# Kernel optimization log

Hardware: AMD Instinct MI355X
Metric: run time of the kernel (lower is better)

Reference implementation:

```python
import jax, jax.numpy as jnp
import numpy as np
from jax import lax

DIM, HID, NH, KD, D, WH = 256, 512, 4, 16, 64, 7


def _conv(x, w, pad, groups):
    return lax.conv_general_dilated(
        x, w, (1, 1), [(pad, pad), (pad, pad)],
        dimension_numbers=('NCHW', 'OIHW', 'NCHW'), feature_group_count=groups)


def _conv_bn(x, w, s, b, pad=0, groups=1):
    # Conv2d(bias=False) followed by eval-mode BatchNorm folded to per-channel affine
    y = _conv(x, w, pad, groups)
    return y * s[None, :, None, None] + b[None, :, None, None]


def _ffn(x, w1, s1, b1, w2, s2, b2):
    return _conv_bn(jax.nn.relu(_conv_bn(x, w1, s1, b1)), w2, s2, b2)


def _window(t, c, B, H, W):
    # [B,NH,c,H,W] -> [B,NH,H//WH,W//WH,WH*WH,c]
    t = t.reshape(B, NH, c, H // WH, WH, W // WH, WH)
    t = t.transpose(0, 1, 3, 5, 4, 6, 2)
    return t.reshape(B, NH, H // WH, W // WH, WH * WH, c)


def _local_window_attn(x, qkv_w, qkv_s, qkv_b, dws_w, dws_s, dws_b,
                       proj_w, proj_s, proj_b, pos_emb):
    B, C, H, W = x.shape
    scale = KD ** -0.5
    qkv = _conv_bn(x, qkv_w, qkv_s, qkv_b)          # [B, NH*(2KD+D), H, W]
    qkv = qkv.reshape(B, NH, 2 * KD + D, H, W)
    q, k, v = qkv[:, :, :KD], qkv[:, :, KD:2 * KD], qkv[:, :, 2 * KD:]
    # per-head depthwise 5x5 conv on q
    q = jax.vmap(lambda qi, wi, si, bi: _conv_bn(qi, wi, si, bi, pad=2, groups=KD),
                 in_axes=(1, 0, 0, 0), out_axes=1)(q, dws_w, dws_s, dws_b)
    q = _window(q, KD, B, H, W)
    k = _window(k, KD, B, H, W)
    v = _window(v, D, B, H, W)
    attn = jnp.einsum('bhijqc,bhijkc->bhijqk', q, k) * scale \
        + pos_emb[None, :, None, None]               # [B,NH,nWh,nWw,Ws,Ws]
    attn = jax.nn.softmax(attn, axis=-1)
    o = jnp.einsum('bhijqk,bhijkd->bhijqd', attn, v)
    o = o.reshape(B, NH, H // WH, W // WH, WH, WH, D)
    o = o.transpose(0, 1, 6, 2, 4, 3, 5).reshape(B, NH * D, H, W)
    return _conv_bn(jax.nn.relu(o), proj_w, proj_s, proj_b)


def setup_inputs() -> dict:
    key = jax.random.key(0)
    ks = iter(jax.random.split(key, 40))
    n = lambda shp, sc=0.05: jax.random.normal(next(ks), shp, jnp.float32) * sc
    u = lambda shp: jax.random.uniform(next(ks), shp, jnp.float32, minval=0.5, maxval=1.5)
    inp = {'x': jax.random.normal(next(ks), (64, DIM, 28, 28), jnp.float32)}
    for p in ('dw0', 'dw1'):
        inp[p + '_w'] = n((DIM, 1, 3, 3))
        inp[p + '_s'] = u((DIM,))
        inp[p + '_b'] = n((DIM,))
    for p in ('ffn0', 'ffn1'):
        inp[p + '_w1'] = n((HID, DIM, 1, 1))
        inp[p + '_s1'] = u((HID,))
        inp[p + '_b1'] = n((HID,))
        inp[p + '_w2'] = n((DIM, HID, 1, 1))
        inp[p + '_s2'] = u((DIM,))
        inp[p + '_b2'] = n((DIM,))
    inp['qkv_w'] = n((NH * (2 * KD + D), DIM, 1, 1))
    inp['qkv_s'] = u((NH * (2 * KD + D),))
    inp['qkv_b'] = n((NH * (2 * KD + D),))
    inp['dws_w'] = n((NH, KD, 1, 5, 5))
    inp['dws_s'] = u((NH, KD))
    inp['dws_b'] = n((NH, KD))
    inp['proj_w'] = n((DIM, NH * D, 1, 1))
    inp['proj_s'] = u((DIM,))
    inp['proj_b'] = n((DIM,))
    inp['pos_emb'] = n((NH, WH * WH, WH * WH))
    return inp


def reference(x, dw0_w, dw0_s, dw0_b,
              ffn0_w1, ffn0_s1, ffn0_b1, ffn0_w2, ffn0_s2, ffn0_b2,
              qkv_w, qkv_s, qkv_b, dws_w, dws_s, dws_b,
              proj_w, proj_s, proj_b, pos_emb,
              dw1_w, dw1_s, dw1_b,
              ffn1_w1, ffn1_s1, ffn1_b1, ffn1_w2, ffn1_s2, ffn1_b2):
    x = x + _conv_bn(x, dw0_w, dw0_s, dw0_b, pad=1, groups=DIM)
    x = x + _ffn(x, ffn0_w1, ffn0_s1, ffn0_b1, ffn0_w2, ffn0_s2, ffn0_b2)
    x = x + _local_window_attn(x, qkv_w, qkv_s, qkv_b, dws_w, dws_s, dws_b,
                               proj_w, proj_s, proj_b, pos_emb)
    x = x + _conv_bn(x, dw1_w, dw1_s, dw1_b, pad=1, groups=DIM)
    x = x + _ffn(x, ffn1_w1, ffn1_s1, ffn1_b1, ffn1_w2, ffn1_s2, ffn1_b2)
    return x
```

## Files before the change

### kernel.cpp

```cpp
#include <hip/hip_runtime.h>
#include <hip/hip_bf16.h>
#include <math.h>

typedef __hip_bfloat16 bf16;
typedef __attribute__((ext_vector_type(8))) short short8;
typedef __attribute__((ext_vector_type(4))) float floatx4;

#define BB    64
#define DIMC  256
#define HIDC  512
#define NHH   4
#define HH_   28
#define WW_   28
#define PP    784

__device__ __forceinline__ float toF(bf16 x) { return __bfloat162float(x); }
__device__ __forceinline__ unsigned short f2bits(float f) {
    union { bf16 h; unsigned short u; } cv; cv.h = __float2bfloat16(f); return cv.u;
}
__device__ __forceinline__ float bits2f(unsigned short u) {
    union { unsigned int u32; float f; } cv; cv.u32 = ((unsigned int)u) << 16; return cv.f;
}

__device__ __forceinline__ void gll16(const void* g, void* l) {
    __builtin_amdgcn_global_load_lds(
        (const __attribute__((address_space(1))) void*)g,
        (__attribute__((address_space(3))) void*)l, 16, 0, 0);
}

__global__ __launch_bounds__(256) void cvt_all(
    const float* __restrict__ s0, bf16* __restrict__ d0,
    const float* __restrict__ s1, bf16* __restrict__ d1,
    const float* __restrict__ s2, bf16* __restrict__ d2,
    const float* __restrict__ s3, bf16* __restrict__ d3,
    const float* __restrict__ s4, bf16* __restrict__ d4,
    const float* __restrict__ s5, bf16* __restrict__ d5)
{
    int i = blockIdx.x * 256 + threadIdx.x;
    if (i < 131072)                d0[i]          = __float2bfloat16(s0[i]);
    else if (i < 262144)           d1[i - 131072] = __float2bfloat16(s1[i - 131072]);
    else if (i < 393216)           d2[i - 262144] = __float2bfloat16(s2[i - 262144]);
    else if (i < 524288)           d3[i - 393216] = __float2bfloat16(s3[i - 393216]);
    else if (i < 622592)           d4[i - 524288] = __float2bfloat16(s4[i - 524288]);
    else if (i < 688128)           d5[i - 622592] = __float2bfloat16(s5[i - 622592]);
}

#define CPB 4
__global__ __launch_bounds__(256) void dw3x3_kernel(
    const float* __restrict__ in, const float* __restrict__ w,
    const float* __restrict__ s, const float* __restrict__ b,
    float* __restrict__ out, bf16* __restrict__ outB)
{
    __shared__ float t[CPB][30 * 30];

    int wid = blockIdx.y * gridDim.x + blockIdx.x;
    int lin = (wid & 7) * 512 + (wid >> 3);
    int cg  = lin & 63;
    int n   = lin >> 6;
    int c0  = cg * CPB;

    int tid = threadIdx.x;
    int lm  = tid & 3;
    const float* ip = in  + ((size_t)n * DIMC + c0) * PP;
    float*       op = out + ((size_t)n * DIMC + c0) * PP;

    float w9[9];
#pragma unroll
    for (int i = 0; i < 9; i++) w9[i] = w[(c0 + lm) * 9 + i];
    float sc = s[c0 + lm], bb = b[c0 + lm];

    for (int i = tid; i < 464; i += 256) {
        int plane = i / 116, bq = i - plane * 116;
        int cell;
        if (bq < 30)       cell = bq;
        else if (bq < 60)  cell = 870 + (bq - 30);
        else if (bq < 88)  cell = (bq - 60 + 1) * 30;
        else               cell = (bq - 88 + 1) * 30 + 29;
        t[plane][cell] = 0.f;
    }
    for (int idx = tid; idx < CPB * 196; idx += 256) {
        int ch  = idx / 196;
        int rm  = idx - ch * 196;
        int row = rm / 7, seg = rm - row * 7;
        float4 v = *(const float4*)&ip[ch * PP + row * 28 + seg * 4];
        float* dst = &t[ch][(row + 1) * 30 + seg * 4 + 1];
        dst[0] = v.x; dst[1] = v.y; dst[2] = v.z; dst[3] = v.w;
    }
    __syncthreads();

    unsigned short* oBu = (unsigned short*)outB;
    for (int idx = tid; idx < CPB * 196; idx += 256) {
        int rm  = idx >> 2;
        int row = rm / 7, seg = rm - row * 7;
        int x0  = seg * 4;

        float acc[4] = {0.f, 0.f, 0.f, 0.f};
        float ctr[4];
        const float* base = &t[lm][row * 30 + x0];
#pragma unroll
        for (int i = 0; i < 3; i++) {
            float r[6];
#pragma unroll
            for (int k = 0; k < 6; k++) r[k] = base[i * 30 + k];
            if (i == 1) { ctr[0] = r[1]; ctr[1] = r[2]; ctr[2] = r[3]; ctr[3] = r[4]; }
#pragma unroll
            for (int j = 0; j < 3; j++)
#pragma unroll
                for (int q = 0; q < 4; q++)
                    acc[q] += w9[i * 3 + j] * r[j + q];
        }
        float v0 = ctr[0] + acc[0] * sc + bb;
        float v1 = ctr[1] + acc[1] * sc + bb;
        float v2 = ctr[2] + acc[2] * sc + bb;
        float v3 = ctr[3] + acc[3] * sc + bb;

        float4 o; o.x = v0; o.y = v1; o.z = v2; o.w = v3;
        *(float4*)&op[lm * PP + row * 28 + x0] = o;

        float ea = __shfl_xor((lm & 2) ? v0 : v2, 2);
        float eb = __shfl_xor((lm & 2) ? v1 : v3, 2);
        v0 = (lm & 2) ? ea : v0;  v1 = (lm & 2) ? eb : v1;
        v2 = (lm & 2) ? v2 : ea;  v3 = (lm & 2) ? v3 : eb;
        float ec = __shfl_xor((lm & 1) ? v0 : v1, 1);
        float ed = __shfl_xor((lm & 1) ? v2 : v3, 1);
        v0 = (lm & 1) ? ec : v0;  v1 = (lm & 1) ? v1 : ec;
        v2 = (lm & 1) ? ed : v2;  v3 = (lm & 1) ? v3 : ed;
        int p = row * 28 + x0 + lm;
        union { unsigned short h[4]; uint2 u; } pk;
        pk.h[0] = f2bits(v0); pk.h[1] = f2bits(v1);
        pk.h[2] = f2bits(v2); pk.h[3] = f2bits(v3);
        *(uint2*)&oBu[((size_t)n * PP + p) * DIMC + c0] = pk.u;
    }
}

__global__ __launch_bounds__(256) void dws5x5_nhwc(
    const bf16* __restrict__ qkv,
    const float* __restrict__ w,
    const float* __restrict__ s, const float* __restrict__ b,
    bf16* __restrict__ qout)
{
    __shared__ __align__(16) unsigned short qin[32 * 32 * 16];
    int hh  = blockIdx.x;
    int n   = blockIdx.y;
    int tid = threadIdx.x;
    const unsigned short* KVu = (const unsigned short*)qkv;

    int kcw = tid & 15;
    int hk  = hh * 16 + kcw;
    float w25[25];
#pragma unroll
    for (int i = 0; i < 25; i++) w25[i] = w[hk * 25 + i];
    float csc = s[hk], cbb = b[hk];

    for (int i = tid; i < 4096; i += 256)
        ((uint4*)qin)[i] = make_uint4(0u, 0u, 0u, 0u);
    __syncthreads();
    for (int idx = tid; idx < 1568; idx += 256) {
        int p = idx >> 1, half = idx & 1;
        int h = p / 28, x = p - h * 28;
        uint4 v = *(const uint4*)&KVu[((size_t)n * PP + p) * 384 + hh * 96 + half * 8];
        *(uint4*)&qin[((h + 2) * 32 + (x + 2)) * 16 + half * 8] = v;
    }
    __syncthreads();

    for (int idx = tid; idx < 12544; idx += 256) {
        int p = idx >> 4;
        int h = p / 28, x = p - h * 28;
        float acc = 0.f;
#pragma unroll
        for (int i = 0; i < 5; i++)
#pragma unroll
            for (int j = 0; j < 5; j++)
                acc += w25[i * 5 + j] * bits2f(qin[((h + i) * 32 + (x + j)) * 16 + kcw]);
        qout[((size_t)n * PP + p) * 64 + hk] = __float2bfloat16(acc * csc + cbb);
    }
}

template <bool RELU, bool RES, int OUTMODE>
__global__ __launch_bounds__(256) void gemm_mfma(
    const bf16* __restrict__ Wb,
    const bf16* __restrict__ X,
    const float* __restrict__ S, const float* __restrict__ Bb,
    const float* __restrict__ res,
    float* __restrict__ outF,
    bf16*  __restrict__ outB,
    int M, int K)
{
    int nwg = gridDim.x * gridDim.y * gridDim.z;
    int wid = (blockIdx.z * gridDim.y + blockIdx.y) * gridDim.x + blockIdx.x;
    int lin = (wid & 7) * (nwg >> 3) + (wid >> 3);
    int yb  = lin % gridDim.y;
    int t2  = lin / gridDim.y;
    int xb  = t2 % gridDim.x;
    int n   = t2 / gridDim.x;

    int co0  = yb * 64;
    int p0   = xb * 112;
    int tid  = threadIdx.x;
    int wv   = tid >> 6;
    int ln   = tid & 63;
    int l15  = ln & 15;
    int quad = ln >> 4;

    __shared__ __align__(16) unsigned short Blds[2][112 * 32];

    floatx4 acc[7];
#pragma unroll
    for (int t = 0; t < 7; t++) acc[t] = (floatx4){0.f, 0.f, 0.f, 0.f};

    const bf16* Arow = Wb + (size_t)(co0 + wv * 16 + l15) * K + quad * 8;
    const unsigned short* Xb = (const unsigned short*)X + ((size_t)n * PP + p0) * K;

    int rA = wv * 16 + (ln >> 2);
    int rB = 64 + wv * 16 + (ln >> 2);
    int cA = (ln & 3) ^ ((rA >> 1) & 3);
    int cB = (ln & 3) ^ ((rB >> 1) & 3);
    const unsigned short* gA = Xb + (size_t)rA * K + cA * 8;
    const unsigned short* gB = Xb + (size_t)rB * K + cB * 8;

    gll16(gA, &Blds[0][(wv * 16) * 32]);
    if (wv < 3) gll16(gB, &Blds[0][(64 + wv * 16) * 32]);
    short8 af = *(const short8*)Arow;
    __syncthreads();

    int NT = K >> 5;
    for (int t = 0; t < NT; t++) {
        int cur = t & 1;
        short8 naf = af;
        if (t + 1 < NT) {
            gll16(gA + (t + 1) * 32, &Blds[cur ^ 1][(wv * 16) * 32]);
            if (wv < 3) gll16(gB + (t + 1) * 32, &Blds[cur ^ 1][(64 + wv * 16) * 32]);
            naf = *(const short8*)(Arow + (t + 1) * 32);
        }
#pragma unroll
        for (int tt = 0; tt < 7; tt++) {
            int row = tt * 16 + l15;
            short8 bfrag = *(const short8*)
                &Blds[cur][row * 32 + ((quad ^ ((row >> 1) & 3)) * 8)];
            acc[tt] = __builtin_amdgcn_mfma_f32_16x16x32_bf16(af, bfrag, acc[tt], 0, 0, 0);
        }
        af = naf;
        __syncthreads();
    }

    int cobase = co0 + wv * 16 + quad * 4;
    float s4[4], b4[4];
#pragma unroll
    for (int r = 0; r < 4; r++) { s4[r] = S[cobase + r]; b4[r] = Bb[cobase + r]; }

#pragma unroll
    for (int t = 0; t < 7; t++) {
        int p = p0 + t * 16 + l15;
        float y[4];
#pragma unroll
        for (int r = 0; r < 4; r++) {
            y[r] = acc[t][r] * s4[r] + b4[r];
            if (RELU) y[r] = fmaxf(y[r], 0.f);
            if (RES) y[r] += res[((size_t)n * M + cobase + r) * PP + p];
        }
        if (OUTMODE == 1 || OUTMODE == 2) {
#pragma unroll
            for (int r = 0; r < 4; r++)
                outF[((size_t)n * M + cobase + r) * PP + p] = y[r];
        }
        if (OUTMODE == 0 || OUTMODE == 2) {
            union { unsigned short h4[4]; uint2 u; } pk;
#pragma unroll
            for (int r = 0; r < 4; r++) pk.h4[r] = f2bits(y[r]);
            *(uint2*)((unsigned short*)outB + ((size_t)n * PP + p) * M + cobase) = pk.u;
        }
    }
}

__global__ __launch_bounds__(256) void attn_kernel(
    const bf16*  __restrict__ Q,
    const bf16*  __restrict__ KV,
    const float* __restrict__ pos,
    bf16* __restrict__ O)
{
    int wjp = blockIdx.x & 1, wi = blockIdx.x >> 1;
    int hh  = blockIdx.y, n = blockIdx.z;
    int tid = threadIdx.x;
    int pbase = wi * 7 * 28 + wjp * 14;

    __shared__ __align__(16) char smem[51712];
    unsigned short* qS = (unsigned short*)smem;
    unsigned short* kS = qS + 2 * 64 * 40;
    unsigned short* pS = (unsigned short*)smem;
    unsigned short* vT = (unsigned short*)(smem + 20480);
    float*          posL = (float*)(smem + 20480 + 18432);

    const unsigned short* Qu  = (const unsigned short*)Q;
    const unsigned short* KVu = (const unsigned short*)KV;

    for (int idx = tid; idx < 1280; idx += 256) {
        int which = idx >= 640 ? 1 : 0;
        int t2 = idx - which * 640;
        int w = t2 / 320, rm = t2 - w * 320;
        int row = rm / 5, half = rm - row * 5;
        uint4 v = make_uint4(0u, 0u, 0u, 0u);
        if (row < 49 && half < 2) {
            int p = pbase + (row / 7) * 28 + w * 7 + (row % 7);
            const unsigned short* src = which
                ? &KVu[((size_t)n * PP + p) * 384 + hh * 96 + 16 + half * 8]
                : &Qu[((size_t)n * PP + p) * 64 + hh * 16 + half * 8];
            v = *(const uint4*)src;
        }
        *(uint4*)((which ? kS : qS) + (w * 64 + row) * 40 + half * 8) = v;
    }
    for (int idx = tid; idx < 1024; idx += 256) {
        int w = idx >> 9, rm = idx & 511;
        int ki = rm >> 3, dq = rm & 7;
        union { uint4 q; unsigned short h[8]; } v;
        v.q = make_uint4(0u, 0u, 0u, 0u);
        if (ki < 49) {
            int p = pbase + (ki / 7) * 28 + w * 7 + (ki % 7);
            v.q = *(const uint4*)&KVu[((size_t)n * PP + p) * 384 + hh * 96 + 32 + dq * 8];
        }
#pragma unroll
        for (int j = 0; j < 8; j++)
            vT[(w * 64 + dq * 8 + j) * 72 + ki] = v.h[j];
    }
    for (int idx = tid; idx < 3200; idx += 256) {
        int r = idx / 50, c = idx - r * 50;
        posL[idx] = (r < 49 && c < 49) ? pos[((size_t)hh * 49 + r) * 49 + c] : 0.f;
    }
    __syncthreads();

    int wv = tid >> 6, ln = tid & 63, l15 = ln & 15, quad = ln >> 4;

    uint2 pk[2][4];
#pragma unroll
    for (int w = 0; w < 2; w++) {
        short8 qf = *(const short8*)&qS[(w * 64 + wv * 16 + l15) * 40 + quad * 8];
        floatx4 a4[4];
#pragma unroll
        for (int kt = 0; kt < 4; kt++) {
            short8 kf = *(const short8*)&kS[(w * 64 + kt * 16 + l15) * 40 + quad * 8];
            a4[kt] = __builtin_amdgcn_mfma_f32_16x16x32_bf16(
                kf, qf, (floatx4){0.f, 0.f, 0.f, 0.f}, 0, 0, 0);
        }
        int q = wv * 16 + l15;
        float sv[16];
        float m = -1e30f;
#pragma unroll
        for (int kt = 0; kt < 4; kt++) {
#pragma unroll
            for (int r = 0; r < 4; r++) {
                int ki = kt * 16 + quad * 4 + r;
                float sc = (ki < 49)
                    ? a4[kt][r] * 0.25f + posL[q * 50 + ki]
                    : -1e30f;
                sv[kt * 4 + r] = sc;
                m = fmaxf(m, sc);
            }
        }
        m = fmaxf(m, __shfl_xor(m, 16));
        m = fmaxf(m, __shfl_xor(m, 32));
        float sum = 0.f;
#pragma unroll
        for (int i = 0; i < 16; i++) { sv[i] = __expf(sv[i] - m); sum += sv[i]; }
        sum += __shfl_xor(sum, 16);
        sum += __shfl_xor(sum, 32);
        float inv = 1.f / sum;
#pragma unroll
        for (int kt = 0; kt < 4; kt++) {
            union { uint2 u; unsigned short h[4]; } pku;
#pragma unroll
            for (int r = 0; r < 4; r++) pku.h[r] = f2bits(sv[kt * 4 + r] * inv);
            pk[w][kt] = pku.u;
        }
    }
    __syncthreads();

    {
        int q = wv * 16 + l15;
#pragma unroll
        for (int w = 0; w < 2; w++)
#pragma unroll
            for (int kt = 0; kt < 4; kt++)
                *(uint2*)&pS[(w * 64 + q) * 72 + kt * 16 + quad * 4] = pk[w][kt];
    }
    __syncthreads();

    unsigned short* Ou = (unsigned short*)O;
#pragma unroll
    for (int w = 0; w < 2; w++) {
        short8 af0 = *(const short8*)&pS[(w * 64 + wv * 16 + l15) * 72 + quad * 8];
        short8 af1 = *(const short8*)&pS[(w * 64 + wv * 16 + l15) * 72 + 32 + quad * 8];
#pragma unroll
        for (int dt = 0; dt < 4; dt++) {
            floatx4 oacc = (floatx4){0.f, 0.f, 0.f, 0.f};
            short8 vf0 = *(const short8*)&vT[(w * 64 + dt * 16 + l15) * 72 + quad * 8];
            short8 vf1 = *(const short8*)&vT[(w * 64 + dt * 16 + l15) * 72 + 32 + quad * 8];
            oacc = __builtin_amdgcn_mfma_f32_16x16x32_bf16(af0, vf0, oacc, 0, 0, 0);
            oacc = __builtin_amdgcn_mfma_f32_16x16x32_bf16(af1, vf1, oacc, 0, 0, 0);
#pragma unroll
            for (int r = 0; r < 4; r++) {
                int q = wv * 16 + quad * 4 + r;
                if (q < 49) {
                    int p = pbase + (q / 7) * 28 + w * 7 + (q % 7);
                    Ou[((size_t)n * PP + p) * 256 + hh * 64 + dt * 16 + l15] =
                        f2bits(fmaxf(oacc[r], 0.f));
                }
            }
        }
    }
}

extern "C" void kernel_launch(void* const* d_in, const int* in_sizes, int n_in,
                              void* d_out, int out_size, void* d_ws, size_t ws_size,
                              hipStream_t stream)
{
    const float* x0     = (const float*)d_in[0];
    const float* dw0_w  = (const float*)d_in[1];
    const float* dw0_s  = (const float*)d_in[2];
    const float* dw0_b  = (const float*)d_in[3];
    const float* dw1_w  = (const float*)d_in[4];
    const float* dw1_s  = (const float*)d_in[5];
    const float* dw1_b  = (const float*)d_in[6];
    const float* f0w1   = (const float*)d_in[7];
    const float* f0s1   = (const float*)d_in[8];
    const float* f0b1   = (const float*)d_in[9];
    const float* f0w2   = (const float*)d_in[10];
    const float* f0s2   = (const float*)d_in[11];
    const float* f0b2   = (const float*)d_in[12];
    const float* f1w1   = (const float*)d_in[13];
    const float* f1s1   = (const float*)d_in[14];
    const float* f1b1   = (const float*)d_in[15];
    const float* f1w2   = (const float*)d_in[16];
    const float* f1s2   = (const float*)d_in[17];
    const float* f1b2   = (const float*)d_in[18];
    const float* qkv_w  = (const float*)d_in[19];
    const float* qkv_s  = (const float*)d_in[20];
    const float* qkv_b  = (const float*)d_in[21];
    const float* dws_w  = (const float*)d_in[22];
    const float* dws_s  = (const float*)d_in[23];
    const float* dws_b  = (const float*)d_in[24];
    const float* proj_w = (const float*)d_in[25];
    const float* proj_s = (const float*)d_in[26];
    const float* proj_b = (const float*)d_in[27];
    const float* pos    = (const float*)d_in[28];

    const size_t NXB = (size_t)BB * DIMC * PP * 4;
    char* base  = (char*)d_ws;
    float* X1   = (float*)base;
    bf16*  Hb   = (bf16*)(base + NXB);
    bf16*  Qb   = Hb;
    char*  C_   = base + 2 * NXB;
    bf16*  QKVb = (bf16*)C_;
    float* X2   = (float*)C_;
    bf16*  X1b  = (bf16*)(base + 3 * NXB);
    bf16*  Wc   = (bf16*)(base + 3 * NXB + NXB / 2);
    bf16*  Ob   = (bf16*)d_out;
    float* outp = (float*)d_out;

    bf16* Wf0w1 = Wc;
    bf16* Wf0w2 = Wf0w1 + 131072;
    bf16* Wf1w1 = Wf0w2 + 131072;
    bf16* Wf1w2 = Wf1w1 + 131072;
    bf16* Wqkv  = Wf1w2 + 131072;
    bf16* Wproj = Wqkv + 98304;

    dim3 blk(256);

    cvt_all<<<2688, blk, 0, stream>>>(f0w1, Wf0w1, f0w2, Wf0w2,
                                      f1w1, Wf1w1, f1w2, Wf1w2,
                                      qkv_w, Wqkv, proj_w, Wproj);

    dw3x3_kernel<<<dim3(DIMC / CPB, BB), blk, 0, stream>>>(
        x0, dw0_w, dw0_s, dw0_b, X1, X1b);

    gemm_mfma<true, false, 0><<<dim3(7, HIDC / 64, BB), blk, 0, stream>>>(
        Wf0w1, X1b, f0s1, f0b1, nullptr, nullptr, Hb, HIDC, DIMC);
    gemm_mfma<false, true, 2><<<dim3(7, DIMC / 64, BB), blk, 0, stream>>>(
        Wf0w2, Hb, f0s2, f0b2, X1, X1, X1b, DIMC, HIDC);

    gemm_mfma<false, false, 0><<<dim3(7, 384 / 64, BB), blk, 0, stream>>>(
        Wqkv, X1b, qkv_s, qkv_b, nullptr, nullptr, QKVb, 384, DIMC);
    dws5x5_nhwc<<<dim3(NHH, BB), blk, 0, stream>>>(QKVb, dws_w, dws_s, dws_b, Qb);
    attn_kernel<<<dim3(8, NHH, BB), blk, 0, stream>>>(Qb, QKVb, pos, Ob);
    gemm_mfma<false, true, 1><<<dim3(7, DIMC / 64, BB), blk, 0, stream>>>(
        Wproj, Ob, proj_s, proj_b, X1, X1, nullptr, DIMC, DIMC);

    dw3x3_kernel<<<dim3(DIMC / CPB, BB), blk, 0, stream>>>(
        X1, dw1_w, dw1_s, dw1_b, X2, X1b);

    gemm_mfma<true, false, 0><<<dim3(7, HIDC / 64, BB), blk, 0, stream>>>(
        Wf1w1, X1b, f1s1, f1b1, nullptr, nullptr, Hb, HIDC, DIMC);
    gemm_mfma<false, true, 1><<<dim3(7, DIMC / 64, BB), blk, 0, stream>>>(
        Wf1w2, Hb, f1s2, f1b2, X2, outp, nullptr, DIMC, HIDC);
}
```

Measured before the change: 463.8 us.

## Carry residual stream in bf16 and drop redundant fp32 residual writes

GEMM epilogues can now read the residual from the bf16 NHWC copy (RESMODE 2) instead of the fp32 NCHW tensor. The depthwise 3x3 kernel gains a template flag that skips its fp32 output store. The first FFN's second GEMM now updates X1b in place with no fp32 copy, and the X2 buffer is removed. This cuts fp32 residual traffic in a memory-bound block, at the cost of rounding the residual path to bf16 at several stages.

```diff
diff --git a/kernel.cpp b/kernel.cpp
--- a/kernel.cpp
+++ b/kernel.cpp
@@ -46,6 +46,7 @@
 }
 
 #define CPB 4
+template <bool WF>
 __global__ __launch_bounds__(256) void dw3x3_kernel(
     const float* __restrict__ in, const float* __restrict__ w,
     const float* __restrict__ s, const float* __restrict__ b,
@@ -114,8 +115,10 @@
         float v2 = ctr[2] + acc[2] * sc + bb;
         float v3 = ctr[3] + acc[3] * sc + bb;
 
-        float4 o; o.x = v0; o.y = v1; o.z = v2; o.w = v3;
-        *(float4*)&op[lm * PP + row * 28 + x0] = o;
+        if (WF) {
+            float4 o; o.x = v0; o.y = v1; o.z = v2; o.w = v3;
+            *(float4*)&op[lm * PP + row * 28 + x0] = o;
+        }
 
         float ea = __shfl_xor((lm & 2) ? v0 : v2, 2);
         float eb = __shfl_xor((lm & 2) ? v1 : v3, 2);
@@ -176,12 +179,13 @@
     }
 }
 
-template <bool RELU, bool RES, int OUTMODE>
+template <bool RELU, int RESMODE, int OUTMODE>
 __global__ __launch_bounds__(256) void gemm_mfma(
     const bf16* __restrict__ Wb,
     const bf16* __restrict__ X,
     const float* __restrict__ S, const float* __restrict__ Bb,
-    const float* __restrict__ res,
+    const float* __restrict__ resF,
+    const bf16*  __restrict__ resB,
     float* __restrict__ outF,
     bf16*  __restrict__ outB,
     int M, int K)
@@ -251,12 +255,25 @@
 #pragma unroll
     for (int t = 0; t < 7; t++) {
         int p = p0 + t * 16 + l15;
+        float resv[4] = {0.f, 0.f, 0.f, 0.f};
+        if (RESMODE == 1) {
+#pragma unroll
+            for (int r = 0; r < 4; r++)
+                resv[r] = resF[((size_t)n * M + cobase + r) * PP + p];
+        }
+        if (RESMODE == 2) {
+            union { uint2 u; unsigned short h[4]; } rr;
+            rr.u = *(const uint2*)((const unsigned short*)resB +
+                                   ((size_t)n * PP + p) * M + cobase);
+#pragma unroll
+            for (int r = 0; r < 4; r++) resv[r] = bits2f(rr.h[r]);
+        }
         float y[4];
 #pragma unroll
         for (int r = 0; r < 4; r++) {
             y[r] = acc[t][r] * s4[r] + b4[r];
             if (RELU) y[r] = fmaxf(y[r], 0.f);
-            if (RES) y[r] += res[((size_t)n * M + cobase + r) * PP + p];
+            if (RESMODE != 0) y[r] += resv[r];
         }
         if (OUTMODE == 1 || OUTMODE == 2) {
 #pragma unroll
@@ -449,7 +466,6 @@
     bf16*  Qb   = Hb;
     char*  C_   = base + 2 * NXB;
     bf16*  QKVb = (bf16*)C_;
-    float* X2   = (float*)C_;
     bf16*  X1b  = (bf16*)(base + 3 * NXB);
     bf16*  Wc   = (bf16*)(base + 3 * NXB + NXB / 2);
     bf16*  Ob   = (bf16*)d_out;
@@ -468,26 +484,26 @@
                                       f1w1, Wf1w1, f1w2, Wf1w2,
                                       qkv_w, Wqkv, proj_w, Wproj);
 
-    dw3x3_kernel<<<dim3(DIMC / CPB, BB), blk, 0, stream>>>(
+    dw3x3_kernel<false><<<dim3(DIMC / CPB, BB), blk, 0, stream>>>(
         x0, dw0_w, dw0_s, dw0_b, X1, X1b);
 
-    gemm_mfma<true, false, 0><<<dim3(7, HIDC / 64, BB), blk, 0, stream>>>(
-        Wf0w1, X1b, f0s1, f0b1, nullptr, nullptr, Hb, HIDC, DIMC);
-    gemm_mfma<false, true, 2><<<dim3(7, DIMC / 64, BB), blk, 0, stream>>>(
-        Wf0w2, Hb, f0s2, f0b2, X1, X1, X1b, DIMC, HIDC);
-
-    gemm_mfma<false, false, 0><<<dim3(7, 384 / 64, BB), blk, 0, stream>>>(
-        Wqkv, X1b, qkv_s, qkv_b, nullptr, nullptr, QKVb, 384, DIMC);
+    gemm_mfma<true, 0, 0><<<dim3(7, HIDC / 64, BB), blk, 0, stream>>>(
+        Wf0w1, X1b, f0s1, f0b1, nullptr, nullptr, nullptr, Hb, HIDC, DIMC);
+    gemm_mfma<false, 2, 0><<<dim3(7, DIMC / 64, BB), blk, 0, stream>>>(
+        Wf0w2, Hb, f0s2, f0b2, nullptr, X1b, nullptr, X1b, DIMC, HIDC);
+
+    gemm_mfma<false, 0, 0><<<dim3(7, 384 / 64, BB), blk, 0, stream>>>(
+        Wqkv, X1b, qkv_s, qkv_b, nullptr, nullptr, nullptr, QKVb, 384, DIMC);
     dws5x5_nhwc<<<dim3(NHH, BB), blk, 0, stream>>>(QKVb, dws_w, dws_s, dws_b, Qb);
     attn_kernel<<<dim3(8, NHH, BB), blk, 0, stream>>>(Qb, QKVb, pos, Ob);
-    gemm_mfma<false, true, 1><<<dim3(7, DIMC / 64, BB), blk, 0, stream>>>(
-        Wproj, Ob, proj_s, proj_b, X1, X1, nullptr, DIMC, DIMC);
-
-    dw3x3_kernel<<<dim3(DIMC / CPB, BB), blk, 0, stream>>>(
-        X1, dw1_w, dw1_s, dw1_b, X2, X1b);
-
-    gemm_mfma<true, false, 0><<<dim3(7, HIDC / 64, BB), blk, 0, stream>>>(
-        Wf1w1, X1b, f1s1, f1b1, nullptr, nullptr, Hb, HIDC, DIMC);
-    gemm_mfma<false, true, 1><<<dim3(7, DIMC / 64, BB), blk, 0, stream>>>(
-        Wf1w2, Hb, f1s2, f1b2, X2, outp, nullptr, DIMC, HIDC);
-}
+    gemm_mfma<false, 2, 1><<<dim3(7, DIMC / 64, BB), blk, 0, stream>>>(
+        Wproj, Ob, proj_s, proj_b, nullptr, X1b, X1, nullptr, DIMC, DIMC);
+
+    dw3x3_kernel<false><<<dim3(DIMC / CPB, BB), blk, 0, stream>>>(
+        X1, dw1_w, dw1_s, dw1_b, X1, X1b);
+
+    gemm_mfma<true, 0, 0><<<dim3(7, HIDC / 64, BB), blk, 0, stream>>>(
+        Wf1w1, X1b, f1s1, f1b1, nullptr, nullptr, nullptr, Hb, HIDC, DIMC);
+    gemm_mfma<false, 2, 1><<<dim3(7, DIMC / 64, BB), blk, 0, stream>>>(
+        Wf1w2, Hb, f1s2, f1b2, nullptr, X1b, outp, nullptr, DIMC, HIDC);
+}
```

Result: faster. 446.1 us (-3.8%).
